# Performance work log

Measured on AMD Instinct MI355X. Metric: run time of the kernel, lower is better.

The kernel has to match this reference:

```python
import jax, jax.numpy as jnp
import numpy as np

# Dims: batch, seq, model dim, heads, routes-per-query, bleed-over alpha
B, S, D, H, K_ROUTES = 4, 512, 1024, 16, 64
HD = D // H                      # head_dim = 64
SCALE = 1.0 / float(np.sqrt(HD))
ALPHA = 0.25                     # neighbor bleed-over (forward arg default 0.0; >0 here)
CAUSAL = True
NEG = jnp.float32(-1e9)


def _build_routes(seq_len: int, k: int, depth: int = 8) -> np.ndarray:
    """Cantor-coordinate based positional routes (mirrors _build_positional_routes)."""
    pos = np.arange(seq_len, dtype=np.float64)
    x = pos / max(1, seq_len - 1)
    x = np.clip(x, 1e-6, 1.0 - 1e-6)
    val = np.zeros_like(x)
    factor = 0.5
    for _ in range(depth):
        xs = x * 3.0
        digit = xs.astype(np.int64)
        frac = xs - digit
        val = val + (digit == 2).astype(np.float64) * factor
        x = frac
        factor *= 0.5
    coords = np.clip(val, 0.0, 1.0)
    dist = np.abs(coords[:, None] - coords[None, :])            # [S,S]
    routes = np.argsort(dist, axis=1, kind='stable')[:, :k]     # k smallest distances
    return routes.astype(np.int32)


def setup_inputs() -> dict:
    key = jax.random.key(0)
    k0, k1, k2 = jax.random.split(key, 3)
    x = jax.random.normal(k0, (B, S, D), dtype=jnp.float32)
    # nn.Linear weights stored pre-transposed as [in, out] for clean matmul
    w_qkv = jax.random.normal(k1, (D, 3 * D), dtype=jnp.float32) * (1.0 / np.sqrt(D))
    b_qkv = jnp.zeros((3 * D,), dtype=jnp.float32)
    w_out = jax.random.normal(k2, (D, D), dtype=jnp.float32) * (1.0 / np.sqrt(D))
    b_out = jnp.zeros((D,), dtype=jnp.float32)
    routes = jnp.asarray(_build_routes(S, K_ROUTES), dtype=jnp.int32)  # [S, K]
    return {"x": x, "w_qkv": w_qkv, "b_qkv": b_qkv,
            "w_out": w_out, "b_out": b_out, "routes": routes}


def reference(x, w_qkv, b_qkv, w_out, b_out, routes):
    # QKV projection: [B,S,3D] -> [3,B,H,S,hd]
    qkv = (x @ w_qkv + b_qkv).reshape(B, S, 3, H, HD).transpose(2, 0, 3, 1, 4)
    q, k, v = qkv[0], qkv[1], qkv[2]                 # each [B,H,S,hd]

    r = routes                                        # [S,K]
    k_g = jnp.take(k, r, axis=2)                      # [B,H,S,K,hd]
    v_g = jnp.take(v, r, axis=2)
    if ALPHA > 0.0:
        rl = jnp.clip(r - 1, 0, S - 1)
        rr = jnp.clip(r + 1, 0, S - 1)
        k_g = (1.0 - ALPHA) * k_g + (ALPHA / 2.0) * (jnp.take(k, rl, axis=2) + jnp.take(k, rr, axis=2))
        v_g = (1.0 - ALPHA) * v_g + (ALPHA / 2.0) * (jnp.take(v, rl, axis=2) + jnp.take(v, rr, axis=2))

    scores = jnp.einsum('bhqd,bhqkd->bhqk', q, k_g) * SCALE   # [B,H,S,K]
    if CAUSAL:
        # route index > query position is masked (each query always routes to itself)
        mask = r > jnp.arange(S, dtype=r.dtype)[:, None]       # [S,K]
        scores = jnp.where(mask[None, None], NEG, scores)

    attn = jax.nn.softmax(scores, axis=-1)
    out = jnp.einsum('bhqk,bhqkd->bhqd', attn, v_g)            # [B,H,S,hd]
    out = out.transpose(0, 2, 1, 3).reshape(B, S, D)
    return out @ w_out + b_out
```

## Files before the change

kernel.cpp:

```cpp
#include <hip/hip_runtime.h>
#include <hip/hip_bf16.h>

#define BB 4
#define SS 512
#define DD 1024
#define HH 16
#define KR 64
#define HDIM 64
#define THREE_D 3072
#define M_ROWS 2048
#define SCALE_F 0.125f
#define SCALE_LOG2E 0.1803368801111144f

typedef __attribute__((ext_vector_type(8))) short short8;
typedef __attribute__((ext_vector_type(4))) float floatx4;

union F8 { short8 s; unsigned int u[4]; unsigned short h[8]; };

__device__ inline float bfu(unsigned short h){ union{unsigned int u; float f;} c; c.u = ((unsigned int)h) << 16; return c.f; }
__device__ inline unsigned short f2bf(float f){
    union{float f; unsigned int u;} c; c.f = f;
    unsigned int u = c.u;
    return (unsigned short)((u + 0x7fffu + ((u >> 16) & 1u)) >> 16);
}

#define GLOAD_LDS16(g, l)                                                     \
    __builtin_amdgcn_global_load_lds(                                         \
        (const __attribute__((address_space(1))) unsigned int*)(g),           \
        (__attribute__((address_space(3))) unsigned int*)(l), 16, 0, 0)

__global__ __launch_bounds__(256) void prep_kernel(
    const float* __restrict__ x, const float* __restrict__ w_qkv,
    const float* __restrict__ w_out, const int* __restrict__ routes,
    unsigned short* __restrict__ xb_sw, unsigned short* __restrict__ wb1_sw,
    unsigned short* __restrict__ wb2_sw, unsigned int* __restrict__ maskg)
{
    const int bx = blockIdx.x;
    const int tid = threadIdx.x;
    if (bx < 1024) {
        int gid = bx * 256 + tid;
        int r  = gid & 127;
        int c  = (gid >> 7) & 3;
        int kt = (gid >> 9) & 31;
        int mt = gid >> 14;
        const float* src = x + ((size_t)(mt * 128 + r)) * 1024 + kt * 32 + c * 8;
        float4 a = *(const float4*)src;
        float4 b = *(const float4*)(src + 4);
        F8 o;
        o.h[0] = f2bf(a.x); o.h[1] = f2bf(a.y); o.h[2] = f2bf(a.z); o.h[3] = f2bf(a.w);
        o.h[4] = f2bf(b.x); o.h[5] = f2bf(b.y); o.h[6] = f2bf(b.z); o.h[7] = f2bf(b.w);
        *(uint4*)(xb_sw + (size_t)gid * 8) = *(uint4*)&o;
    } else if (bx < 3072) {
        const float* w;
        unsigned short* out;
        int gid, N;
        if (bx < 2560) { w = w_qkv; out = wb1_sw; N = THREE_D; gid = (bx - 1024) * 256 + tid; }
        else           { w = w_out; out = wb2_sw; N = DD;      gid = (bx - 2560) * 256 + tid; }
        int r  = gid & 127;
        int c  = (gid >> 7) & 3;
        int kt = (gid >> 9) & 31;
        int nt = gid >> 14;
        int n = nt * 128 + r;
        int kbase = kt * 32 + c * 8;
        F8 o;
#pragma unroll
        for (int j = 0; j < 8; ++j)
            o.h[j] = f2bf(w[(size_t)(kbase + j) * N + n]);
        *(uint4*)(out + (size_t)gid * 8) = *(uint4*)&o;
    } else {
        int q = (bx - 3072) * 256 + tid;
        unsigned int w[16];
#pragma unroll
        for (int i = 0; i < 16; ++i) w[i] = 0u;
        for (int j = 0; j < KR; ++j) {
            int r = routes[q * KR + j];
            if (r <= q) w[r >> 5] |= 1u << (r & 31);
        }
#pragma unroll
        for (int sw = 0; sw < 16; ++sw) maskg[sw * SS + q] = w[sw];
    }
}

__global__ __launch_bounds__(256) void gemm_qkv(
    const unsigned short* __restrict__ Asw,
    const unsigned short* __restrict__ Bsw,
    const float* __restrict__ bias,
    unsigned short* __restrict__ qb, unsigned short* __restrict__ kb,
    unsigned short* __restrict__ vb)
{
    __shared__ __align__(16) unsigned short Sh[24576];
    unsigned short* Alds = Sh;
    unsigned short* Blds = Sh + 8192;

    const int tid  = threadIdx.x;
    const int lane = tid & 63;
    const int wid  = tid >> 6;
    const int l15  = lane & 15;
    const int quad = lane >> 4;

    const int bid  = blockIdx.x;
    const int xcd  = bid & 7;
    const int loc  = bid >> 3;
    const int mt64 = (xcd & 3) * 8 + (loc & 7);
    const int nt   = (xcd >> 2) * 12 + (loc >> 3);

    const int mt = mt64 >> 1;
    const int rh = (mt64 & 1) * 64;
    const int wn = wid * 32;

    floatx4 acc[4][2];
#pragma unroll
    for (int i = 0; i < 4; ++i)
#pragma unroll
        for (int j = 0; j < 2; ++j) acc[i][j] = (floatx4){0.f, 0.f, 0.f, 0.f};

    for (int kt8 = 0; kt8 < 8; ++kt8) {
#pragma unroll
        for (int kh = 0; kh < 4; ++kh) {
            int kt = kt8 * 4 + kh;
            const unsigned short* ga = Asw + ((size_t)(mt * 32 + kt) * 4 + wid) * 1024 + (rh + lane) * 8;
            const unsigned short* gb = Bsw + (size_t)(nt * 32 + kt) * 4096 + wid * 1024 + lane * 8;
            GLOAD_LDS16(ga,       Alds + kh * 2048 + wid * 512 + lane * 8);
            GLOAD_LDS16(gb,       Blds + kh * 4096 + wid * 1024 + lane * 8);
            GLOAD_LDS16(gb + 512, Blds + kh * 4096 + wid * 1024 + 512 + lane * 8);
        }
        __syncthreads();

#pragma unroll
        for (int kh = 0; kh < 4; ++kh) {
            F8 af[4], bf[2];
#pragma unroll
            for (int mi = 0; mi < 4; ++mi)
                af[mi] = *(const F8*)(Alds + kh * 2048 + (size_t)(quad * 64 + mi * 16 + l15) * 8);
#pragma unroll
            for (int ni = 0; ni < 2; ++ni)
                bf[ni] = *(const F8*)(Blds + kh * 4096 + (size_t)(quad * 128 + wn + ni * 16 + l15) * 8);
#pragma unroll
            for (int mi = 0; mi < 4; ++mi)
#pragma unroll
                for (int ni = 0; ni < 2; ++ni)
                    acc[mi][ni] = __builtin_amdgcn_mfma_f32_16x16x32_bf16(
                        af[mi].s, bf[ni].s, acc[mi][ni], 0, 0, 0);
        }
        __syncthreads();
    }

    const int m0 = mt64 * 64;
    const int n0 = nt * 128;

#pragma unroll
    for (int mi = 0; mi < 4; ++mi) {
#pragma unroll
        for (int ni = 0; ni < 2; ++ni) {
            int col = wn + ni * 16 + l15;
            float bv = bias[n0 + col];
#pragma unroll
            for (int r = 0; r < 4; ++r) {
                int row = mi * 16 + quad * 4 + r;
                Sh[row * 136 + col] = f2bf(acc[mi][ni][r] + bv);
            }
        }
    }
    __syncthreads();

    for (int i = tid; i < 1024; i += 256) {
        int rr = i >> 4, cc = i & 15;
        int grow = m0 + rr, gcol = n0 + cc * 8;
        int b = grow >> 9, s = grow & 511;
        int which = gcol >> 10, rem = gcol & 1023;
        int h = rem >> 6, hd = rem & 63;
        unsigned short* dst = (which == 0) ? qb : (which == 1) ? kb : vb;
        uint4 val = *(const uint4*)(Sh + rr * 136 + cc * 8);
        *(uint4*)(dst + (((size_t)(b * HH + h) * SS) + s) * HDIM + hd) = val;
    }
}

__global__ __launch_bounds__(256) void gemm_out(
    const unsigned short* __restrict__ Asw,
    const unsigned short* __restrict__ Bsw,
    const float* __restrict__ bias,
    float* __restrict__ Cout)
{
    __shared__ __align__(16) unsigned short Alds[8192];
    __shared__ __align__(16) unsigned short Blds[8192];

    const int tid  = threadIdx.x;
    const int lane = tid & 63;
    const int wid  = tid >> 6;
    const int l15  = lane & 15;
    const int quad = lane >> 4;

    const int bid  = blockIdx.x;
    const int xcd  = bid & 7;
    const int loc  = bid >> 3;
    const int mt64 = (xcd & 3) * 8 + (loc & 7);
    const int nt64 = (xcd >> 2) * 8 + (loc >> 3);

    const int mt  = mt64 >> 1;
    const int rh  = (mt64 & 1) * 64;
    const int ntB = nt64 >> 1;
    const int rhB = (nt64 & 1) * 64;
    const int wm  = (wid >> 1) * 32;
    const int wn  = (wid & 1) * 32;

    floatx4 acc[2][2];
#pragma unroll
    for (int i = 0; i < 2; ++i)
#pragma unroll
        for (int j = 0; j < 2; ++j) acc[i][j] = (floatx4){0.f, 0.f, 0.f, 0.f};

    for (int kt4 = 0; kt4 < 8; ++kt4) {
#pragma unroll
        for (int kh = 0; kh < 4; ++kh) {
            int kt = kt4 * 4 + kh;
            const unsigned short* ga = Asw + ((size_t)(mt  * 32 + kt) * 4 + wid) * 1024 + (rh  + lane) * 8;
            const unsigned short* gb = Bsw + ((size_t)(ntB * 32 + kt) * 4 + wid) * 1024 + (rhB + lane) * 8;
            GLOAD_LDS16(ga, Alds + kh * 2048 + wid * 512 + lane * 8);
            GLOAD_LDS16(gb, Blds + kh * 2048 + wid * 512 + lane * 8);
        }
        __syncthreads();

#pragma unroll
        for (int kh = 0; kh < 4; ++kh) {
            F8 af[2], bf[2];
#pragma unroll
            for (int mi = 0; mi < 2; ++mi)
                af[mi] = *(const F8*)(Alds + kh * 2048 + (size_t)(quad * 64 + wm + mi * 16 + l15) * 8);
#pragma unroll
            for (int ni = 0; ni < 2; ++ni)
                bf[ni] = *(const F8*)(Blds + kh * 2048 + (size_t)(quad * 64 + wn + ni * 16 + l15) * 8);
#pragma unroll
            for (int mi = 0; mi < 2; ++mi)
#pragma unroll
                for (int ni = 0; ni < 2; ++ni)
                    acc[mi][ni] = __builtin_amdgcn_mfma_f32_16x16x32_bf16(
                        af[mi].s, bf[ni].s, acc[mi][ni], 0, 0, 0);
        }
        __syncthreads();
    }

    const int m0 = mt64 * 64;
    const int n0 = nt64 * 64;
#pragma unroll
    for (int mi = 0; mi < 2; ++mi) {
#pragma unroll
        for (int ni = 0; ni < 2; ++ni) {
            int col = n0 + wn + ni * 16 + l15;
            float bv = bias[col];
#pragma unroll
            for (int r = 0; r < 4; ++r) {
                int row = m0 + wm + mi * 16 + quad * 4 + r;
                Cout[(size_t)row * DD + col] = acc[mi][ni][r] + bv;
            }
        }
    }
}

__global__ __launch_bounds__(256) void blend_kv_kernel(
    const unsigned short* __restrict__ kb, const unsigned short* __restrict__ vb,
    unsigned short* __restrict__ K2g, unsigned short* __restrict__ Vtg)
{
    __shared__ float vt[130][65];
    const int bh = blockIdx.x >> 2;
    const int qd = blockIdx.x & 3;
    const int s0 = qd * 128;
    const int tid = threadIdx.x;
    const unsigned short* kbase = kb + (size_t)bh * SS * HDIM;
    const unsigned short* vbase = vb + (size_t)bh * SS * HDIM;
    unsigned short* Kq = K2g + ((size_t)(bh * 4 + qd)) * 8192;
    unsigned short* Vq = Vtg + ((size_t)(bh * 4 + qd)) * 8192;

    for (int i = tid; i < 130 * 8; i += 256) {
        int row = i >> 3, c8 = (i & 7) << 3;
        int s = s0 + row - 1; s = s < 0 ? 0 : (s > SS - 1 ? SS - 1 : s);
        F8 vv = *(const F8*)(vbase + (size_t)s * 64 + c8);
#pragma unroll
        for (int j = 0; j < 8; ++j) vt[row][c8 + j] = bfu(vv.h[j]);
    }

    for (int i = tid; i < 1024; i += 256) {
        int sl = i >> 3, cc = i & 7;
        int s = s0 + sl;
        int sm = s ? s - 1 : 0;
        int sp = (s < SS - 1) ? s + 1 : SS - 1;
        F8 k0 = *(const F8*)(kbase + (size_t)s  * 64 + cc * 8);
        F8 km = *(const F8*)(kbase + (size_t)sm * 64 + cc * 8);
        F8 kp = *(const F8*)(kbase + (size_t)sp * 64 + cc * 8);
        F8 o;
#pragma unroll
        for (int j = 0; j < 8; ++j)
            o.h[j] = f2bf(0.75f * bfu(k0.h[j]) + 0.125f * (bfu(km.h[j]) + bfu(kp.h[j])));
        *(uint4*)(Kq + (size_t)(sl * 8 + (cc ^ (sl & 7))) * 8) = *(uint4*)&o;
    }
    __syncthreads();

    for (int i = tid; i < 1024; i += 256) {
        int d = i >> 4, scl = i & 15;
        F8 o;
#pragma unroll
        for (int a = 0; a < 8; ++a) {
            int rl = scl * 8 + a;
            o.h[a] = f2bf(0.75f * vt[rl + 1][d] + 0.125f * (vt[rl][d] + vt[rl + 2][d]));
        }
        int chunk = d * 16 + (scl & 8) + ((scl ^ d) & 7);
        *(uint4*)(Vq + (size_t)chunk * 8) = *(uint4*)&o;
    }
}

__global__ __launch_bounds__(256) void attn_kernel(
    const unsigned short* __restrict__ qb,
    const unsigned short* __restrict__ K2g,
    const unsigned short* __restrict__ Vtg,
    const unsigned int* __restrict__ maskg,
    unsigned short* __restrict__ attn_sw)
{
    __shared__ __align__(16) unsigned short Ks2[2][8192];
    __shared__ __align__(16) unsigned short Vs2[2][8192];
    __shared__ __align__(16) unsigned short Ps[4096];

    const int bid = blockIdx.x;
    const int xcd = bid & 7;
    const int loc = bid >> 3;
    const int bh  = xcd * 8 + (loc & 7);
    const int qt8 = loc >> 3;
    const int qt  = (qt8 < 4) ? qt8 : 11 - qt8;
    const int b = bh >> 4, h = bh & 15;
    const int tid  = threadIdx.x;
    const int lane = tid & 63;
    const int wid  = tid >> 6;
    const int l15  = lane & 15;
    const int quad = lane >> 4;

    const int nq    = (qt >> 1) + 1;
    const int qmaxw = qt * 64 + wid * 16 + 15;

    const unsigned short* Kbh = K2g + (size_t)bh * 4 * 8192;
    const unsigned short* Vbh = Vtg + (size_t)bh * 4 * 8192;

    #define STAGE(qd, bufi) do {                                              \
        const unsigned short* kq = Kbh + (size_t)(qd) * 8192 + wid * 2048;    \
        const unsigned short* vq = Vbh + (size_t)(qd) * 8192 + wid * 2048;    \
        unsigned short* kl = Ks2[bufi] + wid * 2048;                          \
        unsigned short* vl = Vs2[bufi] + wid * 2048;                          \
        GLOAD_LDS16(kq + lane * 8,        kl + lane * 8);                     \
        GLOAD_LDS16(kq + 512 + lane * 8,  kl + 512 + lane * 8);               \
        GLOAD_LDS16(kq + 1024 + lane * 8, kl + 1024 + lane * 8);              \
        GLOAD_LDS16(kq + 1536 + lane * 8, kl + 1536 + lane * 8);              \
        GLOAD_LDS16(vq + lane * 8,        vl + lane * 8);                     \
        GLOAD_LDS16(vq + 512 + lane * 8,  vl + 512 + lane * 8);               \
        GLOAD_LDS16(vq + 1024 + lane * 8, vl + 1024 + lane * 8);              \
        GLOAD_LDS16(vq + 1536 + lane * 8, vl + 1536 + lane * 8);              \
    } while (0)

    const int q = qt * 64 + wid * 16 + l15;

    F8 qf[2];
    {
        const unsigned short* qrow = qb + ((size_t)bh * SS + q) * 64;
        qf[0] = *(const F8*)(qrow + quad * 8);
        qf[1] = *(const F8*)(qrow + 32 + quad * 8);
    }

    STAGE(0, 0);
    __syncthreads();

    floatx4 accO[4];
#pragma unroll
    for (int dt = 0; dt < 4; ++dt) accO[dt] = (floatx4){0.f, 0.f, 0.f, 0.f};
    float lsum = 0.f;
    unsigned int* Pw = (unsigned int*)Ps + wid * 512;

    for (int qd = 0; qd < nq; ++qd) {
        if (qd + 1 < nq) STAGE(qd + 1, (qd + 1) & 1);
        const unsigned short* Ksb = Ks2[qd & 1];
        const unsigned short* Vsb = Vs2[qd & 1];
        const int sbase128 = qd * 128;

        floatx4 accS[8];
#pragma unroll
        for (int st = 0; st < 8; ++st) {
            if (sbase128 + (st >> 2) * 64 <= qmaxw) {
                int srow = st * 16 + l15;
                const F8 k0 = *(const F8*)(Ksb + (((srow << 3) | ( quad      ^ (srow & 7))) << 3));
                const F8 k1 = *(const F8*)(Ksb + (((srow << 3) | ((4 + quad) ^ (srow & 7))) << 3));
                floatx4 a = (floatx4){0.f, 0.f, 0.f, 0.f};
                a = __builtin_amdgcn_mfma_f32_16x16x32_bf16(k0.s, qf[0].s, a, 0, 0, 0);
                a = __builtin_amdgcn_mfma_f32_16x16x32_bf16(k1.s, qf[1].s, a, 0, 0, 0);
                accS[st] = a;
            }
        }

#pragma unroll
        for (int ch2 = 0; ch2 < 2; ++ch2) {
            if (sbase128 + ch2 * 64 > qmaxw) continue;
            unsigned int mw0 = maskg[(qd * 4 + ch2 * 2) * SS + q];
            unsigned int mw1 = maskg[(qd * 4 + ch2 * 2 + 1) * SS + q];
#pragma unroll
            for (int t = 0; t < 4; ++t) {
                unsigned int mw = (t & 2) ? mw1 : mw0;
                int sbase = (t & 1) * 16 + quad * 4;
                floatx4 a = accS[ch2 * 4 + t];
                float e0 = ((mw >> (sbase + 0)) & 1u) ? exp2f(a[0] * SCALE_LOG2E) : 0.f;
                float e1 = ((mw >> (sbase + 1)) & 1u) ? exp2f(a[1] * SCALE_LOG2E) : 0.f;
                float e2 = ((mw >> (sbase + 2)) & 1u) ? exp2f(a[2] * SCALE_LOG2E) : 0.f;
                float e3 = ((mw >> (sbase + 3)) & 1u) ? exp2f(a[3] * SCALE_LOG2E) : 0.f;
                lsum += (e0 + e1) + (e2 + e3);
                unsigned int w0 = (unsigned int)f2bf(e0) | ((unsigned int)f2bf(e1) << 16);
                unsigned int w1 = (unsigned int)f2bf(e2) | ((unsigned int)f2bf(e3) << 16);
                int off0 = t * 8 + quad * 2;
                int off1 = off0 + 1;
                Pw[l15 * 32 + ((((off0 >> 2) ^ (l15 & 7)) << 2) | (off0 & 3))] = w0;
                Pw[l15 * 32 + ((((off1 >> 2) ^ (l15 & 7)) << 2) | (off1 & 3))] = w1;
            }
            F8 pa[2];
#pragma unroll
            for (int ks = 0; ks < 2; ++ks) {
                int ci = ks * 4 + quad;
                pa[ks] = *(const F8*)((const unsigned short*)(Pw + l15 * 32) +
                                      ((ci ^ (l15 & 7)) << 3));
            }
#pragma unroll
            for (int dt = 0; dt < 4; ++dt) {
                int d = dt * 16 + l15;
#pragma unroll
                for (int ks = 0; ks < 2; ++ks) {
                    int scl = ch2 * 8 + ks * 4 + quad;
                    int chunk = d * 16 + (scl & 8) + ((scl ^ d) & 7);
                    const F8 bv = *(const F8*)(Vsb + ((size_t)chunk << 3));
                    accO[dt] = __builtin_amdgcn_mfma_f32_16x16x32_bf16(pa[ks].s, bv.s, accO[dt], 0, 0, 0);
                }
            }
        }
        __syncthreads();
    }

    lsum += __shfl_xor(lsum, 16);
    lsum += __shfl_xor(lsum, 32);
    float inv = 1.0f / lsum;

    unsigned short* Ow = Ps + wid * 1024;
#pragma unroll
    for (int r = 0; r < 4; ++r) {
        float invr = __shfl(inv, quad * 4 + r);
#pragma unroll
        for (int dt = 0; dt < 4; ++dt)
            Ow[(quad * 4 + r) * 64 + dt * 16 + l15] = f2bf(accO[dt][r] * invr);
    }
#pragma unroll
    for (int i = 0; i < 2; ++i) {
        int ch = i * 64 + lane;
        int qlocal = ch >> 3, j = ch & 7;
        int qq = qt * 64 + wid * 16 + qlocal;
        int mrow = b * SS + qq;
        int mt = mrow >> 7, rr = mrow & 127;
        int kt2 = h * 2 + (j >> 2), c = j & 3;
        size_t gid = (((size_t)(mt * 32 + kt2) * 4 + c) * 128 + rr);
        *(uint4*)(attn_sw + gid * 8) = *(const uint4*)(Ow + qlocal * 64 + j * 8);
    }
    #undef STAGE
}

extern "C" void kernel_launch(void* const* d_in, const int* in_sizes, int n_in,
                              void* d_out, int out_size, void* d_ws, size_t ws_size,
                              hipStream_t stream)
{
    const float* x     = (const float*)d_in[0];
    const float* w_qkv = (const float*)d_in[1];
    const float* b_qkv = (const float*)d_in[2];
    const float* w_out = (const float*)d_in[3];
    const float* b_out = (const float*)d_in[4];
    const int* routes  = (const int*)d_in[5];

    char* w = (char*)d_ws;
    unsigned short* xb_sw  = (unsigned short*)(w);
    unsigned short* wb1_sw = (unsigned short*)(w + (4u  << 20));
    unsigned short* wb2_sw = (unsigned short*)(w + (10u << 20));
    unsigned short* qbuf   = (unsigned short*)(w + (12u << 20));
    unsigned short* kbuf   = (unsigned short*)(w + (16u << 20));
    unsigned short* vbuf   = (unsigned short*)(w + (20u << 20));
    unsigned short* K2g    = (unsigned short*)(w + (24u << 20));
    unsigned short* Vtg    = (unsigned short*)(w + (28u << 20));
    unsigned short* attnsw = (unsigned short*)(w + (32u << 20));
    unsigned int*   maskg  = (unsigned int*)(w + (36u << 20));

    prep_kernel<<<3074, 256, 0, stream>>>(x, w_qkv, w_out, routes,
                                          xb_sw, wb1_sw, wb2_sw, maskg);

    gemm_qkv<<<768, 256, 0, stream>>>(xb_sw, wb1_sw, b_qkv, qbuf, kbuf, vbuf);

    blend_kv_kernel<<<256, 256, 0, stream>>>(kbuf, vbuf, K2g, Vtg);

    attn_kernel<<<512, 256, 0, stream>>>(qbuf, K2g, Vtg, maskg, attnsw);

    gemm_out<<<512, 256, 0, stream>>>(attnsw, wb2_sw, b_out, (float*)d_out);
}
```

Baseline: 141.4 us.

## Fuse five kernel launches into one cooperative persistent kernel with grid syncs

Replaces the five separate launches (prep, QKV GEMM, K/V blend, attention, output GEMM) with one cooperative kernel of 768 blocks that runs each stage in turn, separated by grid.sync(). The goal is to remove launch gaps and per-kernel ramp-up and tail overhead between the short stages. In exchange, every stage is capped at the grid size and launch_bounds(256,3) occupancy, the prep stage loops over its blocks, and each grid-wide barrier waits for the slowest block. If the cooperative launch fails, the code falls back to the original five launches.

```diff
diff --git a/kernel.cpp b/kernel.cpp
--- a/kernel.cpp
+++ b/kernel.cpp
@@ -1,5 +1,8 @@
 #include <hip/hip_runtime.h>
 #include <hip/hip_bf16.h>
+#include <hip/hip_cooperative_groups.h>
+
+namespace cg = cooperative_groups;
 
 #define BB 4
 #define SS 512
@@ -28,6 +31,425 @@
     __builtin_amdgcn_global_load_lds(                                         \
         (const __attribute__((address_space(1))) unsigned int*)(g),           \
         (__attribute__((address_space(3))) unsigned int*)(l), 16, 0, 0)
+
+__global__ __launch_bounds__(256, 3) void mega_kernel(
+    const float* __restrict__ x, const float* __restrict__ w_qkv,
+    const float* __restrict__ b_qkv, const float* __restrict__ w_out,
+    const float* __restrict__ b_out, const int* __restrict__ routes,
+    unsigned short* __restrict__ xb_sw, unsigned short* __restrict__ wb1_sw,
+    unsigned short* __restrict__ wb2_sw, unsigned short* __restrict__ qb,
+    unsigned short* __restrict__ kb, unsigned short* __restrict__ vb,
+    unsigned short* __restrict__ K2g, unsigned short* __restrict__ Vtg,
+    unsigned short* __restrict__ attn_sw, unsigned int* __restrict__ maskg,
+    float* __restrict__ out)
+{
+    __shared__ __align__(16) unsigned char SMEM[49152];
+    cg::grid_group grid = cg::this_grid();
+
+    const int tid  = threadIdx.x;
+    const int lane = tid & 63;
+    const int wid  = tid >> 6;
+    const int l15  = lane & 15;
+    const int quad = lane >> 4;
+
+    for (int bx = blockIdx.x; bx < 3074; bx += 768) {
+        if (bx < 1024) {
+            int gid = bx * 256 + tid;
+            int r  = gid & 127;
+            int c  = (gid >> 7) & 3;
+            int kt = (gid >> 9) & 31;
+            int mt = gid >> 14;
+            const float* src = x + ((size_t)(mt * 128 + r)) * 1024 + kt * 32 + c * 8;
+            float4 a = *(const float4*)src;
+            float4 b = *(const float4*)(src + 4);
+            F8 o;
+            o.h[0] = f2bf(a.x); o.h[1] = f2bf(a.y); o.h[2] = f2bf(a.z); o.h[3] = f2bf(a.w);
+            o.h[4] = f2bf(b.x); o.h[5] = f2bf(b.y); o.h[6] = f2bf(b.z); o.h[7] = f2bf(b.w);
+            *(uint4*)(xb_sw + (size_t)gid * 8) = *(uint4*)&o;
+        } else if (bx < 3072) {
+            const float* w;
+            unsigned short* outp;
+            int gid, N;
+            if (bx < 2560) { w = w_qkv; outp = wb1_sw; N = THREE_D; gid = (bx - 1024) * 256 + tid; }
+            else           { w = w_out; outp = wb2_sw; N = DD;      gid = (bx - 2560) * 256 + tid; }
+            int r  = gid & 127;
+            int c  = (gid >> 7) & 3;
+            int kt = (gid >> 9) & 31;
+            int nt = gid >> 14;
+            int n = nt * 128 + r;
+            int kbase = kt * 32 + c * 8;
+            F8 o;
+#pragma unroll
+            for (int j = 0; j < 8; ++j)
+                o.h[j] = f2bf(w[(size_t)(kbase + j) * N + n]);
+            *(uint4*)(outp + (size_t)gid * 8) = *(uint4*)&o;
+        } else {
+            int q = (bx - 3072) * 256 + tid;
+            unsigned int wv[16];
+#pragma unroll
+            for (int i = 0; i < 16; ++i) wv[i] = 0u;
+            for (int j = 0; j < KR; ++j) {
+                int r = routes[q * KR + j];
+                if (r <= q) wv[r >> 5] |= 1u << (r & 31);
+            }
+#pragma unroll
+            for (int sw = 0; sw < 16; ++sw) maskg[sw * SS + q] = wv[sw];
+        }
+    }
+    grid.sync();
+
+    {
+        unsigned short* Sh   = (unsigned short*)SMEM;
+        unsigned short* Alds = Sh;
+        unsigned short* Blds = Sh + 8192;
+
+        const int bid  = blockIdx.x;
+        const int xcd  = bid & 7;
+        const int loc  = bid >> 3;
+        const int mt64 = (xcd & 3) * 8 + (loc & 7);
+        const int nt   = (xcd >> 2) * 12 + (loc >> 3);
+
+        const int mt = mt64 >> 1;
+        const int rh = (mt64 & 1) * 64;
+        const int wn = wid * 32;
+
+        floatx4 acc[4][2];
+#pragma unroll
+        for (int i = 0; i < 4; ++i)
+#pragma unroll
+            for (int j = 0; j < 2; ++j) acc[i][j] = (floatx4){0.f, 0.f, 0.f, 0.f};
+
+        for (int kt8 = 0; kt8 < 8; ++kt8) {
+#pragma unroll
+            for (int kh = 0; kh < 4; ++kh) {
+                int kt = kt8 * 4 + kh;
+                const unsigned short* ga = xb_sw  + ((size_t)(mt * 32 + kt) * 4 + wid) * 1024 + (rh + lane) * 8;
+                const unsigned short* gb = wb1_sw + (size_t)(nt * 32 + kt) * 4096 + wid * 1024 + lane * 8;
+                GLOAD_LDS16(ga,       Alds + kh * 2048 + wid * 512 + lane * 8);
+                GLOAD_LDS16(gb,       Blds + kh * 4096 + wid * 1024 + lane * 8);
+                GLOAD_LDS16(gb + 512, Blds + kh * 4096 + wid * 1024 + 512 + lane * 8);
+            }
+            __syncthreads();
+
+#pragma unroll
+            for (int kh = 0; kh < 4; ++kh) {
+                F8 af[4], bf[2];
+#pragma unroll
+                for (int mi = 0; mi < 4; ++mi)
+                    af[mi] = *(const F8*)(Alds + kh * 2048 + (size_t)(quad * 64 + mi * 16 + l15) * 8);
+#pragma unroll
+                for (int ni = 0; ni < 2; ++ni)
+                    bf[ni] = *(const F8*)(Blds + kh * 4096 + (size_t)(quad * 128 + wn + ni * 16 + l15) * 8);
+#pragma unroll
+                for (int mi = 0; mi < 4; ++mi)
+#pragma unroll
+                    for (int ni = 0; ni < 2; ++ni)
+                        acc[mi][ni] = __builtin_amdgcn_mfma_f32_16x16x32_bf16(
+                            af[mi].s, bf[ni].s, acc[mi][ni], 0, 0, 0);
+            }
+            __syncthreads();
+        }
+
+        const int m0 = mt64 * 64;
+        const int n0 = nt * 128;
+
+#pragma unroll
+        for (int mi = 0; mi < 4; ++mi) {
+#pragma unroll
+            for (int ni = 0; ni < 2; ++ni) {
+                int col = wn + ni * 16 + l15;
+                float bv = b_qkv[n0 + col];
+#pragma unroll
+                for (int r = 0; r < 4; ++r) {
+                    int row = mi * 16 + quad * 4 + r;
+                    Sh[row * 136 + col] = f2bf(acc[mi][ni][r] + bv);
+                }
+            }
+        }
+        __syncthreads();
+
+        for (int i = tid; i < 1024; i += 256) {
+            int rr = i >> 4, cc = i & 15;
+            int grow = m0 + rr, gcol = n0 + cc * 8;
+            int b = grow >> 9, s = grow & 511;
+            int which = gcol >> 10, rem = gcol & 1023;
+            int h = rem >> 6, hd = rem & 63;
+            unsigned short* dst = (which == 0) ? qb : (which == 1) ? kb : vb;
+            uint4 val = *(const uint4*)(Sh + rr * 136 + cc * 8);
+            *(uint4*)(dst + (((size_t)(b * HH + h) * SS) + s) * HDIM + hd) = val;
+        }
+    }
+    grid.sync();
+
+    {
+        const int u = blockIdx.x;
+        if (u < 256) {
+            const int bh = u >> 2;
+            const int qd = u & 3;
+            const int s0 = qd * 128;
+            const unsigned short* kbase = kb + (size_t)bh * SS * HDIM;
+            unsigned short* Kq = K2g + ((size_t)(bh * 4 + qd)) * 8192;
+
+            for (int i = tid; i < 1024; i += 256) {
+                int sl = i >> 3, cc = i & 7;
+                int s = s0 + sl;
+                int sm = s ? s - 1 : 0;
+                int sp = (s < SS - 1) ? s + 1 : SS - 1;
+                F8 k0 = *(const F8*)(kbase + (size_t)s  * 64 + cc * 8);
+                F8 km = *(const F8*)(kbase + (size_t)sm * 64 + cc * 8);
+                F8 kp = *(const F8*)(kbase + (size_t)sp * 64 + cc * 8);
+                F8 o;
+#pragma unroll
+                for (int j = 0; j < 8; ++j)
+                    o.h[j] = f2bf(0.75f * bfu(k0.h[j]) + 0.125f * (bfu(km.h[j]) + bfu(kp.h[j])));
+                *(uint4*)(Kq + (size_t)(sl * 8 + (cc ^ (sl & 7))) * 8) = *(uint4*)&o;
+            }
+        } else {
+            const int v    = u - 256;
+            const int bh   = v >> 3;
+            const int qd   = (v >> 1) & 3;
+            const int half = v & 1;
+            const int s0   = qd * 128;
+            const unsigned short* vbase = vb + (size_t)bh * SS * HDIM;
+            unsigned short* Vq = Vtg + ((size_t)(bh * 4 + qd)) * 8192;
+            float (*vt)[33] = (float (*)[33])SMEM;
+
+            for (int i = tid; i < 520; i += 256) {
+                int row = i >> 2, cq = i & 3;
+                int s = s0 + row - 1; s = s < 0 ? 0 : (s > SS - 1 ? SS - 1 : s);
+                F8 vv = *(const F8*)(vbase + (size_t)s * 64 + half * 32 + cq * 8);
+#pragma unroll
+                for (int j = 0; j < 8; ++j) vt[row][cq * 8 + j] = bfu(vv.h[j]);
+            }
+            __syncthreads();
+
+            for (int i = tid; i < 512; i += 256) {
+                int dl = i >> 4, scl = i & 15;
+                int d = half * 32 + dl;
+                F8 o;
+#pragma unroll
+                for (int a = 0; a < 8; ++a) {
+                    int rl = scl * 8 + a;
+                    o.h[a] = f2bf(0.75f * vt[rl + 1][dl] + 0.125f * (vt[rl][dl] + vt[rl + 2][dl]));
+                }
+                int chunk = d * 16 + (scl & 8) + ((scl ^ d) & 7);
+                *(uint4*)(Vq + (size_t)chunk * 8) = *(uint4*)&o;
+            }
+        }
+    }
+    grid.sync();
+
+    if (blockIdx.x < 512) {
+        unsigned short* Ks = (unsigned short*)SMEM;
+        unsigned short* Vs = (unsigned short*)SMEM + 8192;
+        unsigned short* Ps = (unsigned short*)SMEM + 16384;
+
+        const int bid = blockIdx.x;
+        const int xcd = bid & 7;
+        const int loc = bid >> 3;
+        const int bh  = xcd * 8 + (loc & 7);
+        const int qt8 = loc >> 3;
+        const int qt  = (qt8 < 4) ? qt8 : 11 - qt8;
+        const int b = bh >> 4, h = bh & 15;
+
+        const int nq    = (qt >> 1) + 1;
+        const int qmaxw = qt * 64 + wid * 16 + 15;
+
+        const unsigned short* Kbh = K2g + (size_t)bh * 4 * 8192;
+        const unsigned short* Vbh = Vtg + (size_t)bh * 4 * 8192;
+
+        #define ASTAGE(qd) do {                                               \
+            const unsigned short* kq = Kbh + (size_t)(qd) * 8192 + wid * 2048; \
+            const unsigned short* vq = Vbh + (size_t)(qd) * 8192 + wid * 2048; \
+            unsigned short* kl = Ks + wid * 2048;                             \
+            unsigned short* vl = Vs + wid * 2048;                             \
+            GLOAD_LDS16(kq + lane * 8,        kl + lane * 8);                 \
+            GLOAD_LDS16(kq + 512 + lane * 8,  kl + 512 + lane * 8);           \
+            GLOAD_LDS16(kq + 1024 + lane * 8, kl + 1024 + lane * 8);          \
+            GLOAD_LDS16(kq + 1536 + lane * 8, kl + 1536 + lane * 8);          \
+            GLOAD_LDS16(vq + lane * 8,        vl + lane * 8);                 \
+            GLOAD_LDS16(vq + 512 + lane * 8,  vl + 512 + lane * 8);           \
+            GLOAD_LDS16(vq + 1024 + lane * 8, vl + 1024 + lane * 8);          \
+            GLOAD_LDS16(vq + 1536 + lane * 8, vl + 1536 + lane * 8);          \
+        } while (0)
+
+        const int q = qt * 64 + wid * 16 + l15;
+
+        F8 qf[2];
+        {
+            const unsigned short* qrow = qb + ((size_t)bh * SS + q) * 64;
+            qf[0] = *(const F8*)(qrow + quad * 8);
+            qf[1] = *(const F8*)(qrow + 32 + quad * 8);
+        }
+
+        floatx4 accO[4];
+#pragma unroll
+        for (int dt = 0; dt < 4; ++dt) accO[dt] = (floatx4){0.f, 0.f, 0.f, 0.f};
+        float lsum = 0.f;
+        unsigned int* Pw = (unsigned int*)Ps + wid * 512;
+
+        for (int qd = 0; qd < nq; ++qd) {
+            ASTAGE(qd);
+            __syncthreads();
+            const unsigned short* Ksb = Ks;
+            const unsigned short* Vsb = Vs;
+            const int sbase128 = qd * 128;
+
+            floatx4 accS[8];
+#pragma unroll
+            for (int st = 0; st < 8; ++st) {
+                if (sbase128 + (st >> 2) * 64 <= qmaxw) {
+                    int srow = st * 16 + l15;
+                    const F8 k0 = *(const F8*)(Ksb + (((srow << 3) | ( quad      ^ (srow & 7))) << 3));
+                    const F8 k1 = *(const F8*)(Ksb + (((srow << 3) | ((4 + quad) ^ (srow & 7))) << 3));
+                    floatx4 a = (floatx4){0.f, 0.f, 0.f, 0.f};
+                    a = __builtin_amdgcn_mfma_f32_16x16x32_bf16(k0.s, qf[0].s, a, 0, 0, 0);
+                    a = __builtin_amdgcn_mfma_f32_16x16x32_bf16(k1.s, qf[1].s, a, 0, 0, 0);
+                    accS[st] = a;
+                }
+            }
+
+#pragma unroll
+            for (int ch2 = 0; ch2 < 2; ++ch2) {
+                if (sbase128 + ch2 * 64 > qmaxw) continue;
+                unsigned int mw0 = maskg[(qd * 4 + ch2 * 2) * SS + q];
+                unsigned int mw1 = maskg[(qd * 4 + ch2 * 2 + 1) * SS + q];
+#pragma unroll
+                for (int t = 0; t < 4; ++t) {
+                    unsigned int mw = (t & 2) ? mw1 : mw0;
+                    int sbase = (t & 1) * 16 + quad * 4;
+                    floatx4 a = accS[ch2 * 4 + t];
+                    float e0 = ((mw >> (sbase + 0)) & 1u) ? exp2f(a[0] * SCALE_LOG2E) : 0.f;
+                    float e1 = ((mw >> (sbase + 1)) & 1u) ? exp2f(a[1] * SCALE_LOG2E) : 0.f;
+                    float e2 = ((mw >> (sbase + 2)) & 1u) ? exp2f(a[2] * SCALE_LOG2E) : 0.f;
+                    float e3 = ((mw >> (sbase + 3)) & 1u) ? exp2f(a[3] * SCALE_LOG2E) : 0.f;
+                    lsum += (e0 + e1) + (e2 + e3);
+                    unsigned int w0 = (unsigned int)f2bf(e0) | ((unsigned int)f2bf(e1) << 16);
+                    unsigned int w1 = (unsigned int)f2bf(e2) | ((unsigned int)f2bf(e3) << 16);
+                    int off0 = t * 8 + quad * 2;
+                    int off1 = off0 + 1;
+                    Pw[l15 * 32 + ((((off0 >> 2) ^ (l15 & 7)) << 2) | (off0 & 3))] = w0;
+                    Pw[l15 * 32 + ((((off1 >> 2) ^ (l15 & 7)) << 2) | (off1 & 3))] = w1;
+                }
+                F8 pa[2];
+#pragma unroll
+                for (int ks = 0; ks < 2; ++ks) {
+                    int ci = ks * 4 + quad;
+                    pa[ks] = *(const F8*)((const unsigned short*)(Pw + l15 * 32) +
+                                          ((ci ^ (l15 & 7)) << 3));
+                }
+#pragma unroll
+                for (int dt = 0; dt < 4; ++dt) {
+                    int d = dt * 16 + l15;
+#pragma unroll
+                    for (int ks = 0; ks < 2; ++ks) {
+                        int scl = ch2 * 8 + ks * 4 + quad;
+                        int chunk = d * 16 + (scl & 8) + ((scl ^ d) & 7);
+                        const F8 bv = *(const F8*)(Vsb + ((size_t)chunk << 3));
+                        accO[dt] = __builtin_amdgcn_mfma_f32_16x16x32_bf16(pa[ks].s, bv.s, accO[dt], 0, 0, 0);
+                    }
+                }
+            }
+            __syncthreads();
+        }
+
+        lsum += __shfl_xor(lsum, 16);
+        lsum += __shfl_xor(lsum, 32);
+        float inv = 1.0f / lsum;
+
+        unsigned short* Ow = Ps + wid * 1024;
+#pragma unroll
+        for (int r = 0; r < 4; ++r) {
+            float invr = __shfl(inv, quad * 4 + r);
+#pragma unroll
+            for (int dt = 0; dt < 4; ++dt)
+                Ow[(quad * 4 + r) * 64 + dt * 16 + l15] = f2bf(accO[dt][r] * invr);
+        }
+#pragma unroll
+        for (int i = 0; i < 2; ++i) {
+            int ch = i * 64 + lane;
+            int qlocal = ch >> 3, j = ch & 7;
+            int qq = qt * 64 + wid * 16 + qlocal;
+            int mrow = b * SS + qq;
+            int mt = mrow >> 7, rr = mrow & 127;
+            int kt2 = h * 2 + (j >> 2), c = j & 3;
+            size_t gid = (((size_t)(mt * 32 + kt2) * 4 + c) * 128 + rr);
+            *(uint4*)(attn_sw + gid * 8) = *(const uint4*)(Ow + qlocal * 64 + j * 8);
+        }
+        #undef ASTAGE
+    }
+    grid.sync();
+
+    if (blockIdx.x < 512) {
+        unsigned short* Alds = (unsigned short*)SMEM;
+        unsigned short* Blds = (unsigned short*)SMEM + 8192;
+
+        const int bid  = blockIdx.x;
+        const int xcd  = bid & 7;
+        const int loc  = bid >> 3;
+        const int mt64 = (xcd & 3) * 8 + (loc & 7);
+        const int nt64 = (xcd >> 2) * 8 + (loc >> 3);
+
+        const int mt  = mt64 >> 1;
+        const int rh  = (mt64 & 1) * 64;
+        const int ntB = nt64 >> 1;
+        const int rhB = (nt64 & 1) * 64;
+        const int wm  = (wid >> 1) * 32;
+        const int wn  = (wid & 1) * 32;
+
+        floatx4 acc[2][2];
+#pragma unroll
+        for (int i = 0; i < 2; ++i)
+#pragma unroll
+            for (int j = 0; j < 2; ++j) acc[i][j] = (floatx4){0.f, 0.f, 0.f, 0.f};
+
+        for (int kt4 = 0; kt4 < 8; ++kt4) {
+#pragma unroll
+            for (int kh = 0; kh < 4; ++kh) {
+                int kt = kt4 * 4 + kh;
+                const unsigned short* ga = attn_sw + ((size_t)(mt  * 32 + kt) * 4 + wid) * 1024 + (rh  + lane) * 8;
+                const unsigned short* gb = wb2_sw  + ((size_t)(ntB * 32 + kt) * 4 + wid) * 1024 + (rhB + lane) * 8;
+                GLOAD_LDS16(ga, Alds + kh * 2048 + wid * 512 + lane * 8);
+                GLOAD_LDS16(gb, Blds + kh * 2048 + wid * 512 + lane * 8);
+            }
+            __syncthreads();
+
+#pragma unroll
+            for (int kh = 0; kh < 4; ++kh) {
+                F8 af[2], bf[2];
+#pragma unroll
+                for (int mi = 0; mi < 2; ++mi)
+                    af[mi] = *(const F8*)(Alds + kh * 2048 + (size_t)(quad * 64 + wm + mi * 16 + l15) * 8);
+#pragma unroll
+                for (int ni = 0; ni < 2; ++ni)
+                    bf[ni] = *(const F8*)(Blds + kh * 2048 + (size_t)(quad * 64 + wn + ni * 16 + l15) * 8);
+#pragma unroll
+                for (int mi = 0; mi < 2; ++mi)
+#pragma unroll
+                    for (int ni = 0; ni < 2; ++ni)
+                        acc[mi][ni] = __builtin_amdgcn_mfma_f32_16x16x32_bf16(
+                            af[mi].s, bf[ni].s, acc[mi][ni], 0, 0, 0);
+            }
+            __syncthreads();
+        }
+
+        const int m0 = mt64 * 64;
+        const int n0 = nt64 * 64;
+#pragma unroll
+        for (int mi = 0; mi < 2; ++mi) {
+#pragma unroll
+            for (int ni = 0; ni < 2; ++ni) {
+                int col = n0 + wn + ni * 16 + l15;
+                float bv = b_out[col];
+#pragma unroll
+                for (int r = 0; r < 4; ++r) {
+                    int row = m0 + wm + mi * 16 + quad * 4 + r;
+                    out[(size_t)row * DD + col] = acc[mi][ni][r] + bv;
+                }
+            }
+        }
+    }
+}
 
 __global__ __launch_bounds__(256) void prep_kernel(
     const float* __restrict__ x, const float* __restrict__ w_qkv,
@@ -482,15 +904,23 @@
     unsigned short* Vtg    = (unsigned short*)(w + (28u << 20));
     unsigned short* attnsw = (unsigned short*)(w + (32u << 20));
     unsigned int*   maskg  = (unsigned int*)(w + (36u << 20));
-
-    prep_kernel<<<3074, 256, 0, stream>>>(x, w_qkv, w_out, routes,
-                                          xb_sw, wb1_sw, wb2_sw, maskg);
-
-    gemm_qkv<<<768, 256, 0, stream>>>(xb_sw, wb1_sw, b_qkv, qbuf, kbuf, vbuf);
-
-    blend_kv_kernel<<<256, 256, 0, stream>>>(kbuf, vbuf, K2g, Vtg);
-
-    attn_kernel<<<512, 256, 0, stream>>>(qbuf, K2g, Vtg, maskg, attnsw);
-
-    gemm_out<<<512, 256, 0, stream>>>(attnsw, wb2_sw, b_out, (float*)d_out);
+    float*          outp   = (float*)d_out;
+
+    void* args[] = { &x, &w_qkv, &b_qkv, &w_out, &b_out, &routes,
+                     &xb_sw, &wb1_sw, &wb2_sw, &qbuf, &kbuf, &vbuf,
+                     &K2g, &Vtg, &attnsw, &maskg, &outp };
+
+    hipError_t err = hipLaunchCooperativeKernel(
+        reinterpret_cast<const void*>(&mega_kernel), dim3(768), dim3(256),
+        args, 0, stream);
+
+    if (err != hipSuccess) {
+        (void)hipGetLastError();
+        prep_kernel<<<3074, 256, 0, stream>>>(x, w_qkv, w_out, routes,
+                                              xb_sw, wb1_sw, wb2_sw, maskg);
+        gemm_qkv<<<768, 256, 0, stream>>>(xb_sw, wb1_sw, b_qkv, qbuf, kbuf, vbuf);
+        blend_kv_kernel<<<256, 256, 0, stream>>>(kbuf, vbuf, K2g, Vtg);
+        attn_kernel<<<512, 256, 0, stream>>>(qbuf, K2g, Vtg, maskg, attnsw);
+        gemm_out<<<512, 256, 0, stream>>>(attnsw, wb2_sw, b_out, outp);
+    }
 }
```

Result: slower. 463.5 us (+227.9%).

## Double-buffer LDS in both GEMMs and hoist attention mask loads

Applied to the files above, without the earlier changes.

Both projection GEMMs move from a load-sync-compute loop to a double-buffered pipeline: the global-to-LDS copy of the next K chunk is issued before computing on the current one. The QKV GEMM halves its stage depth to fit two buffers in the existing shared array, while the output GEMM doubles its LDS footprint. The attention kernel loads all four mask words per tile up front, before the score MFMAs, so their latency overlaps compute. This hides memory latency at the cost of more LDS (possible occupancy loss in gemm_out) and extra loop iterations in gemm_qkv.

```diff
diff --git a/kernel.cpp b/kernel.cpp
--- a/kernel.cpp
+++ b/kernel.cpp
@@ -89,8 +89,6 @@
     unsigned short* __restrict__ vb)
 {
     __shared__ __align__(16) unsigned short Sh[24576];
-    unsigned short* Alds = Sh;
-    unsigned short* Blds = Sh + 8192;
 
     const int tid  = threadIdx.x;
     const int lane = tid & 63;
@@ -114,27 +112,36 @@
 #pragma unroll
         for (int j = 0; j < 2; ++j) acc[i][j] = (floatx4){0.f, 0.f, 0.f, 0.f};
 
-    for (int kt8 = 0; kt8 < 8; ++kt8) {
-#pragma unroll
-        for (int kh = 0; kh < 4; ++kh) {
-            int kt = kt8 * 4 + kh;
-            const unsigned short* ga = Asw + ((size_t)(mt * 32 + kt) * 4 + wid) * 1024 + (rh + lane) * 8;
-            const unsigned short* gb = Bsw + (size_t)(nt * 32 + kt) * 4096 + wid * 1024 + lane * 8;
-            GLOAD_LDS16(ga,       Alds + kh * 2048 + wid * 512 + lane * 8);
-            GLOAD_LDS16(gb,       Blds + kh * 4096 + wid * 1024 + lane * 8);
-            GLOAD_LDS16(gb + 512, Blds + kh * 4096 + wid * 1024 + 512 + lane * 8);
-        }
-        __syncthreads();
-
-#pragma unroll
-        for (int kh = 0; kh < 4; ++kh) {
+    #define QSTAGE(it, buf) do {                                                          \
+        _Pragma("unroll")                                                                 \
+        for (int kh = 0; kh < 2; ++kh) {                                                  \
+            int kt = (it) * 2 + kh;                                                       \
+            const unsigned short* ga = Asw + ((size_t)(mt * 32 + kt) * 4 + wid) * 1024 + (rh + lane) * 8; \
+            const unsigned short* gb = Bsw + (size_t)(nt * 32 + kt) * 4096 + wid * 1024 + lane * 8;       \
+            GLOAD_LDS16(ga,       Sh + (buf) * 4096 + kh * 2048 + wid * 512 + lane * 8);  \
+            GLOAD_LDS16(gb,       Sh + 8192 + (buf) * 8192 + kh * 4096 + wid * 1024 + lane * 8);          \
+            GLOAD_LDS16(gb + 512, Sh + 8192 + (buf) * 8192 + kh * 4096 + wid * 1024 + 512 + lane * 8);    \
+        }                                                                                 \
+    } while (0)
+
+    QSTAGE(0, 0);
+    __syncthreads();
+
+    for (int it = 0; it < 16; ++it) {
+        const int buf = it & 1;
+        if (it < 15) QSTAGE(it + 1, buf ^ 1);
+
+        const unsigned short* Al = Sh + buf * 4096;
+        const unsigned short* Bl = Sh + 8192 + buf * 8192;
+#pragma unroll
+        for (int kh = 0; kh < 2; ++kh) {
             F8 af[4], bf[2];
 #pragma unroll
             for (int mi = 0; mi < 4; ++mi)
-                af[mi] = *(const F8*)(Alds + kh * 2048 + (size_t)(quad * 64 + mi * 16 + l15) * 8);
+                af[mi] = *(const F8*)(Al + kh * 2048 + (size_t)(quad * 64 + mi * 16 + l15) * 8);
 #pragma unroll
             for (int ni = 0; ni < 2; ++ni)
-                bf[ni] = *(const F8*)(Blds + kh * 4096 + (size_t)(quad * 128 + wn + ni * 16 + l15) * 8);
+                bf[ni] = *(const F8*)(Bl + kh * 4096 + (size_t)(quad * 128 + wn + ni * 16 + l15) * 8);
 #pragma unroll
             for (int mi = 0; mi < 4; ++mi)
 #pragma unroll
@@ -144,6 +151,7 @@
         }
         __syncthreads();
     }
+    #undef QSTAGE
 
     const int m0 = mt64 * 64;
     const int n0 = nt * 128;
@@ -181,8 +189,8 @@
     const float* __restrict__ bias,
     float* __restrict__ Cout)
 {
-    __shared__ __align__(16) unsigned short Alds[8192];
-    __shared__ __align__(16) unsigned short Blds[8192];
+    __shared__ __align__(16) unsigned short Alds[2][8192];
+    __shared__ __align__(16) unsigned short Blds[2][8192];
 
     const int tid  = threadIdx.x;
     const int lane = tid & 63;
@@ -209,26 +217,33 @@
 #pragma unroll
         for (int j = 0; j < 2; ++j) acc[i][j] = (floatx4){0.f, 0.f, 0.f, 0.f};
 
-    for (int kt4 = 0; kt4 < 8; ++kt4) {
-#pragma unroll
-        for (int kh = 0; kh < 4; ++kh) {
-            int kt = kt4 * 4 + kh;
-            const unsigned short* ga = Asw + ((size_t)(mt  * 32 + kt) * 4 + wid) * 1024 + (rh  + lane) * 8;
-            const unsigned short* gb = Bsw + ((size_t)(ntB * 32 + kt) * 4 + wid) * 1024 + (rhB + lane) * 8;
-            GLOAD_LDS16(ga, Alds + kh * 2048 + wid * 512 + lane * 8);
-            GLOAD_LDS16(gb, Blds + kh * 2048 + wid * 512 + lane * 8);
-        }
-        __syncthreads();
+    #define OSTAGE(it, buf) do {                                                          \
+        _Pragma("unroll")                                                                 \
+        for (int kh = 0; kh < 4; ++kh) {                                                  \
+            int kt = (it) * 4 + kh;                                                       \
+            const unsigned short* ga = Asw + ((size_t)(mt  * 32 + kt) * 4 + wid) * 1024 + (rh  + lane) * 8; \
+            const unsigned short* gb = Bsw + ((size_t)(ntB * 32 + kt) * 4 + wid) * 1024 + (rhB + lane) * 8; \
+            GLOAD_LDS16(ga, Alds[buf] + kh * 2048 + wid * 512 + lane * 8);                \
+            GLOAD_LDS16(gb, Blds[buf] + kh * 2048 + wid * 512 + lane * 8);                \
+        }                                                                                 \
+    } while (0)
+
+    OSTAGE(0, 0);
+    __syncthreads();
+
+    for (int it = 0; it < 8; ++it) {
+        const int buf = it & 1;
+        if (it < 7) OSTAGE(it + 1, buf ^ 1);
 
 #pragma unroll
         for (int kh = 0; kh < 4; ++kh) {
             F8 af[2], bf[2];
 #pragma unroll
             for (int mi = 0; mi < 2; ++mi)
-                af[mi] = *(const F8*)(Alds + kh * 2048 + (size_t)(quad * 64 + wm + mi * 16 + l15) * 8);
+                af[mi] = *(const F8*)(Alds[buf] + kh * 2048 + (size_t)(quad * 64 + wm + mi * 16 + l15) * 8);
 #pragma unroll
             for (int ni = 0; ni < 2; ++ni)
-                bf[ni] = *(const F8*)(Blds + kh * 2048 + (size_t)(quad * 64 + wn + ni * 16 + l15) * 8);
+                bf[ni] = *(const F8*)(Blds[buf] + kh * 2048 + (size_t)(quad * 64 + wn + ni * 16 + l15) * 8);
 #pragma unroll
             for (int mi = 0; mi < 2; ++mi)
 #pragma unroll
@@ -238,6 +253,7 @@
         }
         __syncthreads();
     }
+    #undef OSTAGE
 
     const int m0 = mt64 * 64;
     const int n0 = nt64 * 64;
@@ -376,6 +392,10 @@
         const unsigned short* Vsb = Vs2[qd & 1];
         const int sbase128 = qd * 128;
 
+        unsigned int mwv[4];
+#pragma unroll
+        for (int m = 0; m < 4; ++m) mwv[m] = maskg[(qd * 4 + m) * SS + q];
+
         floatx4 accS[8];
 #pragma unroll
         for (int st = 0; st < 8; ++st) {
@@ -393,11 +413,9 @@
 #pragma unroll
         for (int ch2 = 0; ch2 < 2; ++ch2) {
             if (sbase128 + ch2 * 64 > qmaxw) continue;
-            unsigned int mw0 = maskg[(qd * 4 + ch2 * 2) * SS + q];
-            unsigned int mw1 = maskg[(qd * 4 + ch2 * 2 + 1) * SS + q];
 #pragma unroll
             for (int t = 0; t < 4; ++t) {
-                unsigned int mw = (t & 2) ? mw1 : mw0;
+                unsigned int mw = mwv[ch2 * 2 + ((t >> 1) & 1)];
                 int sbase = (t & 1) * 16 + quad * 4;
                 floatx4 a = accS[ch2 * 4 + t];
                 float e0 = ((mw >> (sbase + 0)) & 1u) ? exp2f(a[0] * SCALE_LOG2E) : 0.f;
```

Result: no change. 143.0 us (+1.2%).
